# Kernel tuning notes

Hardware: AMD Instinct MI355X
Metric: run time of the kernel (lower is better)

## Reference

```python
import jax, jax.numpy as jnp
import numpy as np

EPS = 1e-12  # torch spectral_norm default eps


def _l2norm(v):
    return v / (jnp.linalg.norm(v) + EPS)


def _spectral_norm_2d(w, u):
    # one power iteration (torch default n_power_iterations=1), u/v detached
    v = _l2norm(w.T @ u)
    u_new = _l2norm(w @ v)
    u_new = jax.lax.stop_gradient(u_new)
    v = jax.lax.stop_gradient(v)
    sigma = u_new @ (w @ v)
    return w / sigma


def _spectral_norm_1d(b):
    # torch._SpectralNorm for ndim==1: F.normalize(weight, dim=0)
    return b / (jnp.linalg.norm(b) + EPS)


def setup_inputs() -> dict:
    key = jax.random.key(0)
    ks = jax.random.split(key, 8)
    T, B, I, H = 4096, 32, 256, 256
    s_i = 1.0 / np.sqrt(H)  # nn.RNN init: U(-1/sqrt(H), 1/sqrt(H))
    return {
        "x": jax.random.normal(ks[0], (T, B, I), jnp.float32),
        "state": jax.random.normal(ks[1], (1, B, H), jnp.float32),
        "w_ih": jax.random.uniform(ks[2], (H, I), jnp.float32, -s_i, s_i),
        "w_hh": jax.random.uniform(ks[3], (H, H), jnp.float32, -s_i, s_i),
        "b_ih": jax.random.uniform(ks[4], (H,), jnp.float32, -s_i, s_i),
        "b_hh": jax.random.uniform(ks[5], (H,), jnp.float32, -s_i, s_i),
        "u_ih": jax.random.normal(ks[6], (H,), jnp.float32),  # power-iteration buffer
        "u_hh": jax.random.normal(ks[7], (H,), jnp.float32),
    }


def reference(x, state, w_ih, w_hh, b_ih, b_hh, u_ih, u_hh):
    # spectral-norm parametrization of all RNN weights
    w_ih_sn = _spectral_norm_2d(w_ih, _l2norm(u_ih))
    w_hh_sn = _spectral_norm_2d(w_hh, _l2norm(u_hh))
    b_sn = _spectral_norm_1d(b_ih) + _spectral_norm_1d(b_hh)

    # input projection batched over all timesteps: [T,B,H]
    pre = jnp.einsum("tbi,hi->tbh", x, w_ih_sn) + b_sn

    def step(h, p):
        h_new = jnp.tanh(p + h @ w_hh_sn.T)
        return h_new, h_new

    h_last, out = jax.lax.scan(step, state[0], pre)
    return out, h_last[None]
```

## Files before the change

### kernel.cpp

```cpp
#include <hip/hip_runtime.h>
#include <hip/hip_bf16.h>
#include <math.h>

#define EPSF 1e-12f
#define H 256
#define TSTEPS 4096
#define BATCH 32
#define TB (TSTEPS*BATCH)
#define BH (BATCH*H)

typedef _Float16 h2 __attribute__((ext_vector_type(2)));

#if defined(__has_builtin)
#if __has_builtin(__builtin_amdgcn_fdot2)
#define FDOT2(a, b, c) __builtin_amdgcn_fdot2((a), (b), (c), false)
#endif
#endif
#ifndef FDOT2
#define FDOT2(a, b, c) fmaf((float)(a).y, (float)(b).y, fmaf((float)(a).x, (float)(b).x, (c)))
#endif

__device__ __forceinline__ float block_sum256(float v, float* red) {
  #pragma unroll
  for (int o = 32; o > 0; o >>= 1) v += __shfl_down(v, o, 64);
  __syncthreads();
  if ((threadIdx.x & 63) == 0) red[threadIdx.x >> 6] = v;
  __syncthreads();
  return red[0] + red[1] + red[2] + red[3];
}

__global__ __launch_bounds__(256) void k_prep(
    const float* __restrict__ w_ih, const float* __restrict__ w_hh,
    const float* __restrict__ b_ih, const float* __restrict__ b_hh,
    const float* __restrict__ u_ih, const float* __restrict__ u_hh,
    float* __restrict__ wsc) {
  __shared__ float red[4];
  __shared__ float ubuf[H];
  __shared__ float vbuf[H];
  const int tid = threadIdx.x;

  float inv_sig[2];
  const float* Ws[2] = {w_ih, w_hh};
  const float* Us[2] = {u_ih, u_hh};
  #pragma unroll 1
  for (int m = 0; m < 2; m++) {
    const float* W = Ws[m];
    float uv = Us[m][tid];
    float nu = sqrtf(block_sum256(uv * uv, red));
    ubuf[tid] = uv / (nu + EPSF);
    __syncthreads();
    float vt = 0.f;
    for (int h = 0; h < H; h++) vt = fmaf(W[h * H + tid], ubuf[h], vt);
    float nv = sqrtf(block_sum256(vt * vt, red));
    vbuf[tid] = vt / (nv + EPSF);
    __syncthreads();
    float wv = 0.f;
    const float* wr = W + (size_t)tid * H;
    for (int i = 0; i < H; i++) wv = fmaf(wr[i], vbuf[i], wv);
    float n2 = block_sum256(wv * wv, red);
    float sigma = n2 / (sqrtf(n2) + EPSF);
    inv_sig[m] = 1.f / sigma;
  }
  float bi = b_ih[tid], bh = b_hh[tid];
  float nbi = sqrtf(block_sum256(bi * bi, red));
  float nbh = sqrtf(block_sum256(bh * bh, red));
  wsc[tid] = bi / (nbi + EPSF) + bh / (nbh + EPSF);
  if (tid == 0) { wsc[H] = inv_sig[0]; wsc[H + 1] = inv_sig[1]; }
}

__global__ __launch_bounds__(256) void k_pre(
    const float* __restrict__ x, const float* __restrict__ w_ih,
    const float* __restrict__ wsc, float* __restrict__ pre) {
  __shared__ float xs[32 * 256];
  const int tid = threadIdx.x;
  const size_t m0 = (size_t)blockIdx.x * 32;

  const float4* xp = (const float4*)(x + m0 * H);
  float4* xsv = (float4*)xs;
  #pragma unroll
  for (int j = 0; j < 8; j++) xsv[j * 256 + tid] = xp[j * 256 + tid];
  __syncthreads();

  float acc[32];
  #pragma unroll
  for (int m = 0; m < 32; m++) acc[m] = 0.f;

  const float* wrow = w_ih + (size_t)tid * H;
  #pragma unroll 1
  for (int kb = 0; kb < 256; kb += 8) {
    float4 wa = *(const float4*)(wrow + kb);
    float4 wb = *(const float4*)(wrow + kb + 4);
    #pragma unroll
    for (int m = 0; m < 32; m++) {
      const float* xr = xs + m * 256 + kb;
      float4 xa = *(const float4*)xr;
      float4 xb = *(const float4*)(xr + 4);
      float a = acc[m];
      a = fmaf(xa.x, wa.x, a); a = fmaf(xa.y, wa.y, a);
      a = fmaf(xa.z, wa.z, a); a = fmaf(xa.w, wa.w, a);
      a = fmaf(xb.x, wb.x, a); a = fmaf(xb.y, wb.y, a);
      a = fmaf(xb.z, wb.z, a); a = fmaf(xb.w, wb.w, a);
      acc[m] = a;
    }
  }
  const float inv_s = wsc[H];
  const float bsn = wsc[tid];
  #pragma unroll
  for (int m = 0; m < 32; m++)
    pre[(m0 + m) * H + tid] = fmaf(acc[m], inv_s, bsn);
}

__global__ __launch_bounds__(1024, 4) void k_scan(
    const float* __restrict__ state, const float* __restrict__ w_hh,
    const float* __restrict__ wsc, float* __restrict__ out) {
  __shared__ __align__(16) _Float16 hbuf[2][H];
  __shared__ float part[4][H];
  const int tid = threadIdx.x;
  const int cg = tid >> 8;
  const int r  = tid & 255;
  const int b = blockIdx.x;
  const float inv_s = wsc[H + 1];

  h2 wreg[32];
  const float* wr = w_hh + (size_t)r * H + (cg << 6);
  #pragma unroll
  for (int j = 0; j < 16; j++) {
    float4 wv = *(const float4*)(wr + j * 4);
    wreg[2 * j]     = h2{(_Float16)(wv.x * inv_s), (_Float16)(wv.y * inv_s)};
    wreg[2 * j + 1] = h2{(_Float16)(wv.z * inv_s), (_Float16)(wv.w * inv_s)};
  }

  if (tid < H) hbuf[0][tid] = (_Float16)state[b * H + tid];
  float* outb = out + (size_t)b * H + r;
  float pre0 = 0.f, pre1 = 0.f;
  if (cg == 0) { pre0 = outb[0]; pre1 = outb[BH]; }
  __syncthreads();

  float hn = 0.f;
  #pragma unroll 1
  for (int t = 0; t < TSTEPS; t++) {
    float pre2 = 0.f;
    if (cg == 0) {
      int tn = (t + 2 <= TSTEPS) ? (t + 2) : TSTEPS;
      pre2 = outb[(size_t)tn * BH];
    }

    const uint4* hb = (const uint4*)(hbuf[t & 1] + (cg << 6));
    float acc = 0.f;
    #pragma unroll
    for (int j = 0; j < 8; j++) {
      uint4 q = hb[j];
      acc = FDOT2(wreg[4 * j + 0], __builtin_bit_cast(h2, q.x), acc);
      acc = FDOT2(wreg[4 * j + 1], __builtin_bit_cast(h2, q.y), acc);
      acc = FDOT2(wreg[4 * j + 2], __builtin_bit_cast(h2, q.z), acc);
      acc = FDOT2(wreg[4 * j + 3], __builtin_bit_cast(h2, q.w), acc);
    }
    part[cg][r] = acc;
    __syncthreads();

    if (cg == 0) {
      float s = part[0][r] + part[1][r] + part[2][r] + part[3][r] + pre0;
      float sc = fminf(fmaxf(s, -15.f), 15.f);
      float e = __expf(2.f * sc);
      hn = __fdividef(e - 1.f, e + 1.f);
      outb[(size_t)t * BH] = hn;
      hbuf[(t + 1) & 1][r] = (_Float16)hn;
    }
    __syncthreads();
    pre0 = pre1; pre1 = pre2;
  }
  if (cg == 0) out[(size_t)TSTEPS * BH + b * H + r] = hn;
}

extern "C" void kernel_launch(void* const* d_in, const int* in_sizes, int n_in,
                              void* d_out, int out_size, void* d_ws, size_t ws_size,
                              hipStream_t stream) {
  const float* x     = (const float*)d_in[0];
  const float* state = (const float*)d_in[1];
  const float* w_ih  = (const float*)d_in[2];
  const float* w_hh  = (const float*)d_in[3];
  const float* b_ih  = (const float*)d_in[4];
  const float* b_hh  = (const float*)d_in[5];
  const float* u_ih  = (const float*)d_in[6];
  const float* u_hh  = (const float*)d_in[7];
  float* out = (float*)d_out;
  float* wsc = (float*)d_ws;

  k_prep<<<1, 256, 0, stream>>>(w_ih, w_hh, b_ih, b_hh, u_ih, u_hh, wsc);
  k_pre<<<TB / 32, 256, 0, stream>>>(x, w_ih, wsc, out);
  k_scan<<<BATCH, 1024, 0, stream>>>(state, w_hh, wsc, out);
}
```

Measured before the change: 2.860 ms.

## Remap scan threads: 512 threads each computing 4 rows over 32-column slices

The recurrent scan kernel goes from 1024 threads (4 column groups × 256 rows) to 512 threads (8 column groups × 64 threads × 4 rows each). Each thread loads its 32-element hidden slice once and reuses it for four rows, and writes its partial sums with one float4 store. The goal is fewer LDS reads and fewer waves taking part in each per-step barrier. The cost is an 8-way partial reduction instead of 4-way and the same register weight footprint spread over fewer threads.

```diff
diff --git a/kernel.cpp b/kernel.cpp
--- a/kernel.cpp
+++ b/kernel.cpp
@@ -19,6 +19,8 @@
 #ifndef FDOT2
 #define FDOT2(a, b, c) fmaf((float)(a).y, (float)(b).y, fmaf((float)(a).x, (float)(b).x, (c)))
 #endif
+
+#define BC(u) __builtin_bit_cast(h2, (u))
 
 __device__ __forceinline__ float block_sum256(float v, float* red) {
   #pragma unroll
@@ -110,66 +112,86 @@
     pre[(m0 + m) * H + tid] = fmaf(acc[m], inv_s, bsn);
 }
 
-__global__ __launch_bounds__(1024, 4) void k_scan(
+__global__ __launch_bounds__(512, 1) void k_scan(
     const float* __restrict__ state, const float* __restrict__ w_hh,
     const float* __restrict__ wsc, float* __restrict__ out) {
   __shared__ __align__(16) _Float16 hbuf[2][H];
-  __shared__ float part[4][H];
+  __shared__ __align__(16) float part[8][H];
   const int tid = threadIdx.x;
-  const int cg = tid >> 8;
-  const int r  = tid & 255;
+  const int cg = tid >> 6;
+  const int q  = tid & 63;
+  const int r0 = q << 2;
   const int b = blockIdx.x;
   const float inv_s = wsc[H + 1];
 
-  h2 wreg[32];
-  const float* wr = w_hh + (size_t)r * H + (cg << 6);
-  #pragma unroll
-  for (int j = 0; j < 16; j++) {
-    float4 wv = *(const float4*)(wr + j * 4);
-    wreg[2 * j]     = h2{(_Float16)(wv.x * inv_s), (_Float16)(wv.y * inv_s)};
-    wreg[2 * j + 1] = h2{(_Float16)(wv.z * inv_s), (_Float16)(wv.w * inv_s)};
+  h2 wreg[4][16];
+  #pragma unroll
+  for (int i = 0; i < 4; i++) {
+    const float* wr = w_hh + (size_t)(r0 + i) * H + (cg << 5);
+    #pragma unroll
+    for (int c = 0; c < 16; c++) {
+      float2 wv = *(const float2*)(wr + 2 * c);
+      wreg[i][c] = h2{(_Float16)(wv.x * inv_s), (_Float16)(wv.y * inv_s)};
+    }
   }
 
   if (tid < H) hbuf[0][tid] = (_Float16)state[b * H + tid];
-  float* outb = out + (size_t)b * H + r;
+  float* outb = out + (size_t)b * H + tid;
   float pre0 = 0.f, pre1 = 0.f;
-  if (cg == 0) { pre0 = outb[0]; pre1 = outb[BH]; }
+  if (tid < H) { pre0 = outb[0]; pre1 = outb[BH]; }
   __syncthreads();
 
   float hn = 0.f;
   #pragma unroll 1
   for (int t = 0; t < TSTEPS; t++) {
     float pre2 = 0.f;
-    if (cg == 0) {
+    if (tid < H) {
       int tn = (t + 2 <= TSTEPS) ? (t + 2) : TSTEPS;
       pre2 = outb[(size_t)tn * BH];
     }
 
-    const uint4* hb = (const uint4*)(hbuf[t & 1] + (cg << 6));
-    float acc = 0.f;
+    const uint4* hb = (const uint4*)(hbuf[t & 1] + (cg << 5));
+    uint4 q0 = hb[0], q1 = hb[1], q2 = hb[2], q3 = hb[3];
+
+    float acc[4];
     #pragma unroll
-    for (int j = 0; j < 8; j++) {
-      uint4 q = hb[j];
-      acc = FDOT2(wreg[4 * j + 0], __builtin_bit_cast(h2, q.x), acc);
-      acc = FDOT2(wreg[4 * j + 1], __builtin_bit_cast(h2, q.y), acc);
-      acc = FDOT2(wreg[4 * j + 2], __builtin_bit_cast(h2, q.z), acc);
-      acc = FDOT2(wreg[4 * j + 3], __builtin_bit_cast(h2, q.w), acc);
-    }
-    part[cg][r] = acc;
-    __syncthreads();
-
-    if (cg == 0) {
-      float s = part[0][r] + part[1][r] + part[2][r] + part[3][r] + pre0;
+    for (int i = 0; i < 4; i++) {
+      float a = 0.f;
+      a = FDOT2(wreg[i][ 0], BC(q0.x), a);
+      a = FDOT2(wreg[i][ 1], BC(q0.y), a);
+      a = FDOT2(wreg[i][ 2], BC(q0.z), a);
+      a = FDOT2(wreg[i][ 3], BC(q0.w), a);
+      a = FDOT2(wreg[i][ 4], BC(q1.x), a);
+      a = FDOT2(wreg[i][ 5], BC(q1.y), a);
+      a = FDOT2(wreg[i][ 6], BC(q1.z), a);
+      a = FDOT2(wreg[i][ 7], BC(q1.w), a);
+      a = FDOT2(wreg[i][ 8], BC(q2.x), a);
+      a = FDOT2(wreg[i][ 9], BC(q2.y), a);
+      a = FDOT2(wreg[i][10], BC(q2.z), a);
+      a = FDOT2(wreg[i][11], BC(q2.w), a);
+      a = FDOT2(wreg[i][12], BC(q3.x), a);
+      a = FDOT2(wreg[i][13], BC(q3.y), a);
+      a = FDOT2(wreg[i][14], BC(q3.z), a);
+      a = FDOT2(wreg[i][15], BC(q3.w), a);
+      acc[i] = a;
+    }
+    *(float4*)&part[cg][r0] = make_float4(acc[0], acc[1], acc[2], acc[3]);
+    __syncthreads();
+
+    if (tid < H) {
+      float s = pre0;
+      #pragma unroll
+      for (int g = 0; g < 8; g++) s += part[g][tid];
       float sc = fminf(fmaxf(s, -15.f), 15.f);
       float e = __expf(2.f * sc);
       hn = __fdividef(e - 1.f, e + 1.f);
       outb[(size_t)t * BH] = hn;
-      hbuf[(t + 1) & 1][r] = (_Float16)hn;
+      hbuf[(t + 1) & 1][tid] = (_Float16)hn;
     }
     __syncthreads();
     pre0 = pre1; pre1 = pre2;
   }
-  if (cg == 0) out[(size_t)TSTEPS * BH + b * H + r] = hn;
+  if (tid < H) out[(size_t)TSTEPS * BH + b * H + tid] = hn;
 }
 
 extern "C" void kernel_launch(void* const* d_in, const int* in_sizes, int n_in,
@@ -188,5 +210,5 @@
 
   k_prep<<<1, 256, 0, stream>>>(w_ih, w_hh, b_ih, b_hh, u_ih, u_hh, wsc);
   k_pre<<<TB / 32, 256, 0, stream>>>(x, w_ih, wsc, out);
-  k_scan<<<BATCH, 1024, 0, stream>>>(state, w_hh, wsc, out);
-}
+  k_scan<<<BATCH, 512, 0, stream>>>(state, w_hh, wsc, out);
+}
```

After: 2.711 ms. 1.05x faster.
